# Performance work log

Hardware: AMD Instinct MI355X
Metric: run time of the kernel (lower is better)

Reference implementation:

```python
import jax, jax.numpy as jnp
import numpy as np
from jax import lax

# Four fixed 3x3 directional difference kernels, stacked as OIHW [4,1,3,3]
_KL = np.array([[0, 0, 0], [-1, 1, 0], [0, 0, 0]], dtype=np.float32)
_KR = np.array([[0, 0, 0], [0, 1, -1], [0, 0, 0]], dtype=np.float32)
_KU = np.array([[0, -1, 0], [0, 1, 0], [0, 0, 0]], dtype=np.float32)
_KD = np.array([[0, 0, 0], [0, 1, 0], [0, -1, 0]], dtype=np.float32)
DIR_KERNELS = jnp.asarray(np.stack([_KL, _KR, _KU, _KD])[:, None, :, :])  # [4,1,3,3]


def _avg_pool4(x):
    # x: [B,1,H,W] with H,W divisible by 4 -> [B,1,H/4,W/4]
    B, C, H, W = x.shape
    return x.reshape(B, C, H // 4, 4, W // 4, 4).mean(axis=(3, 5))


def _dir_diffs(x):
    # x: [B,1,h,w] -> [B,4,h,w], 3x3 conv with zero padding 1 (SAME)
    return lax.conv_general_dilated(
        x, DIR_KERNELS,
        window_strides=(1, 1), padding=((1, 1), (1, 1)),
        dimension_numbers=('NCHW', 'OIHW', 'NCHW'))


def setup_inputs() -> dict:
    key = jax.random.key(0)
    k1, k2 = jax.random.split(key)
    org = jax.random.uniform(k1, (32, 3, 512, 512), dtype=jnp.float32)
    enhance = jax.random.uniform(k2, (32, 3, 512, 512), dtype=jnp.float32)
    return {"org": org, "enhance": enhance}


def reference(org, enhance):
    org_pool = _avg_pool4(org.mean(axis=1, keepdims=True))          # [B,1,h,w]
    enh_pool = _avg_pool4(enhance.mean(axis=1, keepdims=True))      # [B,1,h,w]
    d = _dir_diffs(org_pool) - _dir_diffs(enh_pool)                  # [B,4,h,w]
    E = jnp.sum(d * d, axis=1, keepdims=True)                        # [B,1,h,w]
    return E
```

## Files before the change

kernel.cpp:

```cpp
#include <hip/hip_runtime.h>


__global__ __launch_bounds__(256) void pool_diff_kernel(
    const float4* __restrict__ org, const float4* __restrict__ enh,
    float* __restrict__ p) {
  int idx = blockIdx.x * 256 + threadIdx.x;
  int px = idx & 127;
  int py = (idx >> 7) & 127;
  int b  = idx >> 14;
  int base = b * 3 * 512 * 128 + py * 4 * 128 + px;
  float sum = 0.f;
#pragma unroll
  for (int c = 0; c < 3; ++c) {
#pragma unroll
    for (int dy = 0; dy < 4; ++dy) {
      int off = base + (c * 512 + dy) * 128;
      float4 o = org[off];
      float4 e = enh[off];
      sum += (o.x - e.x) + (o.y - e.y) + (o.z - e.z) + (o.w - e.w);
    }
  }
  p[idx] = sum * (1.0f / 48.0f);
}

__global__ __launch_bounds__(256) void espa_stencil_kernel(
    const float* __restrict__ p, float* __restrict__ out) {
  int idx = blockIdx.x * 256 + threadIdx.x;
  int x = idx & 127;
  int y = (idx >> 7) & 127;
  float c = p[idx];
  float l = (x > 0)   ? p[idx - 1]   : 0.f;
  float r = (x < 127) ? p[idx + 1]   : 0.f;
  float u = (y > 0)   ? p[idx - 128] : 0.f;
  float d = (y < 127) ? p[idx + 128] : 0.f;
  float dl = c - l, dr = c - r, du = c - u, dd = c - d;
  out[idx] = dl * dl + dr * dr + du * du + dd * dd;
}

extern "C" void kernel_launch(void* const* d_in, const int* in_sizes, int n_in,
                              void* d_out, int out_size, void* d_ws, size_t ws_size,
                              hipStream_t stream) {
  const float4* org = (const float4*)d_in[0];
  const float4* enh = (const float4*)d_in[1];
  float* p   = (float*)d_ws;
  float* out = (float*)d_out;

  const int N = 32 * 128 * 128;
  pool_diff_kernel<<<N / 256, 256, 0, stream>>>(org, enh, p);
  espa_stencil_kernel<<<N / 256, 256, 0, stream>>>(p, out);
}
```

Baseline: 211.8 us.

## Remap pooling kernel to one block per pooled row with shared-memory reduction

Each block now handles one pooled output row: 256 threads each load 4 consecutive float4 rows' worth (two row pairs across 3 channels), then halves are combined through shared memory. Before, each thread strided across 4 input rows with per-warp accesses to contiguous 128-float4 spans. Now a warp reads fully contiguous 256 float4 segments, which is meant to improve coalescing and memory-level parallelism. It adds a __syncthreads and leaves half the threads idle during the final store.

```diff
diff --git a/kernel.cpp b/kernel.cpp
--- a/kernel.cpp
+++ b/kernel.cpp
@@ -4,23 +4,41 @@
 __global__ __launch_bounds__(256) void pool_diff_kernel(
     const float4* __restrict__ org, const float4* __restrict__ enh,
     float* __restrict__ p) {
-  int idx = blockIdx.x * 256 + threadIdx.x;
-  int px = idx & 127;
-  int py = (idx >> 7) & 127;
-  int b  = idx >> 14;
-  int base = b * 3 * 512 * 128 + py * 4 * 128 + px;
-  float sum = 0.f;
-#pragma unroll
-  for (int c = 0; c < 3; ++c) {
-#pragma unroll
-    for (int dy = 0; dy < 4; ++dy) {
-      int off = base + (c * 512 + dy) * 128;
-      float4 o = org[off];
-      float4 e = enh[off];
-      sum += (o.x - e.x) + (o.y - e.y) + (o.z - e.z) + (o.w - e.w);
-    }
+  __shared__ float red[128];
+  int t = threadIdx.x;
+  int s = blockIdx.x;
+  int b = s >> 7;
+  int py = s & 127;
+  int sb = b * 196608 + py * 512;
+
+  int j0 = sb + t;
+  float4 A0 = org[j0];
+  float4 B0 = enh[j0];
+  float4 A1 = org[j0 + 65536];
+  float4 B1 = enh[j0 + 65536];
+  float4 A2 = org[j0 + 131072];
+  float4 B2 = enh[j0 + 131072];
+  float a0 = (A0.x - B0.x) + (A0.y - B0.y) + (A0.z - B0.z) + (A0.w - B0.w)
+           + (A1.x - B1.x) + (A1.y - B1.y) + (A1.z - B1.z) + (A1.w - B1.w)
+           + (A2.x - B2.x) + (A2.y - B2.y) + (A2.z - B2.z) + (A2.w - B2.w);
+
+  int j1 = j0 + 256;
+  float4 C0 = org[j1];
+  float4 D0 = enh[j1];
+  float4 C1 = org[j1 + 65536];
+  float4 D1 = enh[j1 + 65536];
+  float4 C2 = org[j1 + 131072];
+  float4 D2 = enh[j1 + 131072];
+  float a1 = (C0.x - D0.x) + (C0.y - D0.y) + (C0.z - D0.z) + (C0.w - D0.w)
+           + (C1.x - D1.x) + (C1.y - D1.y) + (C1.z - D1.z) + (C1.w - D1.w)
+           + (C2.x - D2.x) + (C2.y - D2.y) + (C2.z - D2.z) + (C2.w - D2.w);
+
+  float mine = a0 + a1;
+  if (t >= 128) red[t - 128] = mine;
+  __syncthreads();
+  if (t < 128) {
+    p[b * 16384 + py * 128 + t] = (mine + red[t]) * (1.0f / 48.0f);
   }
-  p[idx] = sum * (1.0f / 48.0f);
 }
 
 __global__ __launch_bounds__(256) void espa_stencil_kernel(
@@ -45,7 +63,7 @@
   float* p   = (float*)d_ws;
   float* out = (float*)d_out;
 
+  pool_diff_kernel<<<4096, 256, 0, stream>>>(org, enh, p);
   const int N = 32 * 128 * 128;
-  pool_diff_kernel<<<N / 256, 256, 0, stream>>>(org, enh, p);
   espa_stencil_kernel<<<N / 256, 256, 0, stream>>>(p, out);
 }
```

Measured after the change: 210.6 us. About the same (-0.6%).
